# Kernel tuning notes

Measured on AMD Instinct MI355X. Metric: run time of the kernel, lower is better.

## Reference

```python
import jax, jax.numpy as jnp
import numpy as np


def setup_inputs() -> dict:
    key = jax.random.key(0)
    k1, k2, k3 = jax.random.split(key, 3)
    B, C2, H, W = 8, 128, 28, 28   # resnet18 layer2 output for 224x224 input
    C3, H3, W3 = 256, 14, 14       # resnet18 layer3 output
    M = 30000                      # memory bank patches (post-coreset)
    f2 = jax.random.normal(k1, (B, C2, H, W), dtype=jnp.float32)
    f3 = jax.random.normal(k2, (B, C3, H3, W3), dtype=jnp.float32)
    memory_bank = jax.random.normal(k3, (M, C2 + C3), dtype=jnp.float32)
    return {"f2": f2, "f3": f3, "memory_bank": memory_bank}


def reference(f2, f3, memory_bank):
    """PatchCore predict: multi-layer embed + brute-force 1-NN euclidean distance.

    f2: [B,C2,H,W] (layer2 feats), f3: [B,C3,H3,W3] (layer3 feats),
    memory_bank: [M, C2+C3]. Returns (patch_scores [B,H,W], img_scores [B]).
    """
    B, C2, H, W = f2.shape
    C3 = f3.shape[1]
    # F.interpolate(..., mode='bilinear', align_corners=False) == jax.image.resize bilinear
    f3_up = jax.image.resize(f3, (B, C3, H, W), method="bilinear")
    emb = jnp.concatenate([f2, f3_up], axis=1)            # [B,C,H,W], C=C2+C3
    C = C2 + C3
    patches = emb.transpose(0, 2, 3, 1).reshape(-1, C)    # [N,C], N=B*H*W
    x_sq = jnp.sum(patches * patches, axis=-1, keepdims=True)      # [N,1]
    m_sq = jnp.sum(memory_bank * memory_bank, axis=-1)[None, :]    # [1,M]
    d2 = x_sq + m_sq - 2.0 * (patches @ memory_bank.T)             # [N,M]
    dists = jnp.sqrt(jnp.maximum(d2, 1e-12))
    nn_dist = jnp.min(dists, axis=1)                               # 1-NN (n_neighbors=1)
    patch_scores = nn_dist.reshape(B, H, W)
    img_scores = jnp.max(patch_scores.reshape(B, -1), axis=1)
    return patch_scores, img_scores
```

## Files before the change

### kernel.cpp

```cpp
#include <hip/hip_runtime.h>
#include <hip/hip_bf16.h>
#include <stdint.h>

typedef float f32x4 __attribute__((ext_vector_type(4)));
typedef short bf16x8 __attribute__((ext_vector_type(8)));

#define NPATCH 6272
#define CTOT   384
#define MBANK  30000
#define MROWS  6400
#define NCOLS  30208
#define NKT    6

__global__ __launch_bounds__(256) void prep_patches_kernel(
    const float* __restrict__ f2, const float* __restrict__ f3,
    __hip_bfloat16* __restrict__ A, float* __restrict__ x_sq,
    float* __restrict__ nn_d2)
{
  const int lane = threadIdx.x & 63;
  const int n = blockIdx.x * 4 + (threadIdx.x >> 6);
  if (n >= MROWS) return;
  if (n >= NPATCH) {
    #pragma unroll
    for (int j = 0; j < 6; ++j) A[(size_t)n * CTOT + j * 64 + lane] = __float2bfloat16(0.f);
    return;
  }
  const int b = n / 784;
  const int hw = n - b * 784;
  const int h = hw / 28;
  const int w = hw - h * 28;

  int h0, h1, w0i, w1i; float wh0, wh1, ww0, ww1;
  if (h & 1) { int k = h >> 1; h0 = k; h1 = (k + 1 < 14) ? k + 1 : 13; wh0 = 0.75f; wh1 = 0.25f; }
  else       { int k = h >> 1; h0 = (k > 0) ? k - 1 : 0; h1 = k;       wh0 = 0.25f; wh1 = 0.75f; }
  if (w & 1) { int k = w >> 1; w0i = k; w1i = (k + 1 < 14) ? k + 1 : 13; ww0 = 0.75f; ww1 = 0.25f; }
  else       { int k = w >> 1; w0i = (k > 0) ? k - 1 : 0; w1i = k;       ww0 = 0.25f; ww1 = 0.75f; }

  float ssum = 0.f;
  #pragma unroll
  for (int j = 0; j < 6; ++j) {
    const int c = j * 64 + lane;
    float v;
    if (j < 2) {
      v = f2[(((size_t)b * 128 + c) * 28 + h) * 28 + w];
    } else {
      const int c3 = c - 128;
      const float* p = f3 + ((size_t)b * 256 + c3) * 196;
      v = wh0 * (ww0 * p[h0 * 14 + w0i] + ww1 * p[h0 * 14 + w1i]) +
          wh1 * (ww0 * p[h1 * 14 + w0i] + ww1 * p[h1 * 14 + w1i]);
    }
    A[(size_t)n * CTOT + c] = __float2bfloat16(v);
    ssum += v * v;
  }
  #pragma unroll
  for (int off = 32; off; off >>= 1) ssum += __shfl_xor(ssum, off);
  if (lane == 0) { x_sq[n] = ssum; nn_d2[n] = __uint_as_float(0x7f800000u); }
}

__global__ __launch_bounds__(256) void prep_bank_kernel(
    const float* __restrict__ mb, __hip_bfloat16* __restrict__ Bb,
    float* __restrict__ m_sq)
{
  const int lane = threadIdx.x & 63;
  const int m = blockIdx.x * 4 + (threadIdx.x >> 6);
  if (m >= NCOLS) return;
  if (m < MBANK) {
    float ssum = 0.f;
    #pragma unroll
    for (int j = 0; j < 3; ++j) {
      const int c = j * 128 + lane * 2;
      const float2 v = *(const float2*)&mb[(size_t)m * CTOT + c];
      short2 o;
      o.x = (short)__bfloat16_as_ushort(__float2bfloat16(v.x));
      o.y = (short)__bfloat16_as_ushort(__float2bfloat16(v.y));
      *(short2*)&Bb[(size_t)m * CTOT + c] = o;
      ssum += v.x * v.x + v.y * v.y;
    }
    #pragma unroll
    for (int off = 32; off; off >>= 1) ssum += __shfl_xor(ssum, off);
    if (lane == 0) m_sq[m] = ssum;
  } else {
    #pragma unroll
    for (int j = 0; j < 6; ++j) Bb[(size_t)m * CTOT + j * 64 + lane] = __float2bfloat16(0.f);
    if (lane == 0) m_sq[m] = __uint_as_float(0x7f800000u);
  }
}

__device__ __forceinline__ void gl_lds16(const void* g, void* l) {
  __builtin_amdgcn_global_load_lds(
      (const __attribute__((address_space(1))) uint32_t*)g,
      (__attribute__((address_space(3))) uint32_t*)l, 16, 0, 0);
}

__global__ __launch_bounds__(512, 2) void gemm_min_kernel(
    const __hip_bfloat16* __restrict__ A, const __hip_bfloat16* __restrict__ B,
    const float* __restrict__ x_sq, const float* __restrict__ m_sq,
    float* __restrict__ nn_d2)
{
  __shared__ __align__(16) short As[2][256 * 64];
  __shared__ __align__(16) short Bs[2][256 * 64];
  const int tid  = threadIdx.x;
  const int lane = tid & 63;
  const int wid  = tid >> 6;
  const int wr = wid >> 2;
  const int wc = wid & 3;
  const int row0 = blockIdx.y * 256;
  const int col0 = blockIdx.x * 256;

  f32x4 acc[8][4];
  #pragma unroll
  for (int i = 0; i < 8; ++i)
    #pragma unroll
    for (int j = 0; j < 4; ++j) acc[i][j] = (f32x4){0.f, 0.f, 0.f, 0.f};

  auto stage = [&](int kt, int buf) {
    const int k0 = kt * 64;
    #pragma unroll
    for (int j = 0; j < 4; ++j) {
      const int cb = j * 512 + wid * 64;
      const int c  = cb + lane;
      const int r  = c >> 3;
      const int ch = (c & 7) ^ (r & 7);
      gl_lds16(A + (size_t)(row0 + r) * CTOT + k0 + ch * 8, &As[buf][cb * 8]);
      gl_lds16(B + (size_t)(col0 + r) * CTOT + k0 + ch * 8, &Bs[buf][cb * 8]);
    }
  };

  stage(0, 0);
  stage(1, 1);
  asm volatile("s_waitcnt vmcnt(8)" ::: "memory");
  __builtin_amdgcn_s_barrier();

  const int sw = lane & 7;
  const int rA = wr * 128 + (lane & 15);
  const int rB = wc * 64 + (lane & 15);
  const int kq = lane >> 4;

  #pragma unroll
  for (int t = 0; t < NKT; ++t) {
    const int cur = t & 1;
    const short* lA = As[cur];
    const short* lB = Bs[cur];
    const int ch0 = (kq ^ sw) << 4;
    const int ch1 = ((4 + kq) ^ sw) << 4;

    bf16x8 a0[8], b0[4], a1[8], b1[4];
    #pragma unroll
    for (int mi = 0; mi < 8; ++mi)
      a0[mi] = *(const bf16x8*)((const char*)lA + (rA + mi * 16) * 128 + ch0);
    #pragma unroll
    for (int ni = 0; ni < 4; ++ni)
      b0[ni] = *(const bf16x8*)((const char*)lB + (rB + ni * 16) * 128 + ch0);
    #pragma unroll
    for (int mi = 0; mi < 8; ++mi)
      a1[mi] = *(const bf16x8*)((const char*)lA + (rA + mi * 16) * 128 + ch1);
    #pragma unroll
    for (int ni = 0; ni < 4; ++ni)
      b1[ni] = *(const bf16x8*)((const char*)lB + (rB + ni * 16) * 128 + ch1);

    #pragma unroll
    for (int mi = 0; mi < 8; ++mi)
      #pragma unroll
      for (int ni = 0; ni < 4; ++ni)
        acc[mi][ni] = __builtin_amdgcn_mfma_f32_16x16x32_bf16(a0[mi], b0[ni], acc[mi][ni], 0, 0, 0);

    asm volatile("s_waitcnt lgkmcnt(0)" ::: "memory");
    __builtin_amdgcn_s_barrier();
    if (t + 2 < NKT) stage(t + 2, cur);

    __builtin_amdgcn_s_setprio(1);
    #pragma unroll
    for (int mi = 0; mi < 8; ++mi)
      #pragma unroll
      for (int ni = 0; ni < 4; ++ni)
        acc[mi][ni] = __builtin_amdgcn_mfma_f32_16x16x32_bf16(a1[mi], b1[ni], acc[mi][ni], 0, 0, 0);
    __builtin_amdgcn_s_setprio(0);

    if (t + 2 < NKT) {
      asm volatile("s_waitcnt vmcnt(8)" ::: "memory");
    } else {
      asm volatile("s_waitcnt vmcnt(0)" ::: "memory");
    }
    __builtin_amdgcn_s_barrier();
  }

  float msq[4];
  #pragma unroll
  for (int ni = 0; ni < 4; ++ni) msq[ni] = m_sq[col0 + wc * 64 + ni * 16 + (lane & 15)];

  #pragma unroll
  for (int mi = 0; mi < 8; ++mi) {
    #pragma unroll
    for (int r = 0; r < 4; ++r) {
      float t = msq[0] - 2.f * acc[mi][0][r];
      #pragma unroll
      for (int ni = 1; ni < 4; ++ni) t = fminf(t, msq[ni] - 2.f * acc[mi][ni][r]);
      t = fminf(t, __shfl_xor(t, 1));
      t = fminf(t, __shfl_xor(t, 2));
      t = fminf(t, __shfl_xor(t, 4));
      t = fminf(t, __shfl_xor(t, 8));
      if ((lane & 15) == 0) {
        const int rg = row0 + wr * 128 + mi * 16 + ((lane >> 4) << 2) + r;
        if (rg < NPATCH) {
          const float v = fmaxf(t + x_sq[rg], 0.f);
          atomicMin((unsigned int*)&nn_d2[rg], __float_as_uint(v));
        }
      }
    }
  }
}

__global__ __launch_bounds__(256) void finalize_kernel(
    const float* __restrict__ nn_d2, float* __restrict__ out)
{
  const int b = blockIdx.x;
  const int tid = threadIdx.x;
  __shared__ float red[4];
  float lmax = 0.f;
  for (int i = tid; i < 784; i += 256) {
    const float d2 = nn_d2[b * 784 + i];
    const float s = sqrtf(fmaxf(d2, 1e-12f));
    out[b * 784 + i] = s;
    lmax = fmaxf(lmax, s);
  }
  #pragma unroll
  for (int off = 32; off; off >>= 1) lmax = fmaxf(lmax, __shfl_xor(lmax, off));
  if ((tid & 63) == 0) red[tid >> 6] = lmax;
  __syncthreads();
  if (tid == 0)
    out[6272 + b] = fmaxf(fmaxf(red[0], red[1]), fmaxf(red[2], red[3]));
}

extern "C" void kernel_launch(void* const* d_in, const int* in_sizes, int n_in,
                              void* d_out, int out_size, void* d_ws, size_t ws_size,
                              hipStream_t stream)
{
  const float* f2 = (const float*)d_in[0];
  const float* f3 = (const float*)d_in[1];
  const float* mb = (const float*)d_in[2];
  float* out = (float*)d_out;

  uint8_t* ws = (uint8_t*)d_ws;
  __hip_bfloat16* A  = (__hip_bfloat16*)(ws);
  __hip_bfloat16* Bb = (__hip_bfloat16*)(ws + 4915200);
  float* x_sq  = (float*)(ws + 28114944);
  float* m_sq  = (float*)(ws + 28140544);
  float* nn_d2 = (float*)(ws + 28261376);

  hipLaunchKernelGGL(prep_patches_kernel, dim3(MROWS / 4), dim3(256), 0, stream,
                     f2, f3, A, x_sq, nn_d2);
  hipLaunchKernelGGL(prep_bank_kernel, dim3(NCOLS / 4), dim3(256), 0, stream,
                     mb, Bb, m_sq);
  hipLaunchKernelGGL(gemm_min_kernel, dim3(NCOLS / 256, MROWS / 256), dim3(512), 0, stream,
                     A, Bb, x_sq, m_sq, nn_d2);
  hipLaunchKernelGGL(finalize_kernel, dim3(8), dim3(256), 0, stream, nn_d2, out);
}
```

Before: 452.5 us.

## Interleave GEMM tile staging with quarter-phase MFMA blocks and merge prep kernels

```diff
diff --git a/kernel.cpp b/kernel.cpp
--- a/kernel.cpp
+++ b/kernel.cpp
@@ -12,77 +12,78 @@
 #define NCOLS  30208
 #define NKT    6
 
-__global__ __launch_bounds__(256) void prep_patches_kernel(
+#define NPB    (MROWS / 4)
+#define NBB    (NCOLS / 4)
+
+__global__ __launch_bounds__(256) void prep_kernel(
     const float* __restrict__ f2, const float* __restrict__ f3,
-    __hip_bfloat16* __restrict__ A, float* __restrict__ x_sq,
+    const float* __restrict__ mb,
+    __hip_bfloat16* __restrict__ A, __hip_bfloat16* __restrict__ Bb,
+    float* __restrict__ x_sq, float* __restrict__ m_sq,
     float* __restrict__ nn_d2)
 {
   const int lane = threadIdx.x & 63;
-  const int n = blockIdx.x * 4 + (threadIdx.x >> 6);
-  if (n >= MROWS) return;
-  if (n >= NPATCH) {
-    #pragma unroll
-    for (int j = 0; j < 6; ++j) A[(size_t)n * CTOT + j * 64 + lane] = __float2bfloat16(0.f);
-    return;
-  }
-  const int b = n / 784;
-  const int hw = n - b * 784;
-  const int h = hw / 28;
-  const int w = hw - h * 28;
-
-  int h0, h1, w0i, w1i; float wh0, wh1, ww0, ww1;
-  if (h & 1) { int k = h >> 1; h0 = k; h1 = (k + 1 < 14) ? k + 1 : 13; wh0 = 0.75f; wh1 = 0.25f; }
-  else       { int k = h >> 1; h0 = (k > 0) ? k - 1 : 0; h1 = k;       wh0 = 0.25f; wh1 = 0.75f; }
-  if (w & 1) { int k = w >> 1; w0i = k; w1i = (k + 1 < 14) ? k + 1 : 13; ww0 = 0.75f; ww1 = 0.25f; }
-  else       { int k = w >> 1; w0i = (k > 0) ? k - 1 : 0; w1i = k;       ww0 = 0.25f; ww1 = 0.75f; }
-
-  float ssum = 0.f;
-  #pragma unroll
-  for (int j = 0; j < 6; ++j) {
-    const int c = j * 64 + lane;
-    float v;
-    if (j < 2) {
-      v = f2[(((size_t)b * 128 + c) * 28 + h) * 28 + w];
+  const int sub  = threadIdx.x >> 6;
+
+  if (blockIdx.x < NPB) {
+    const int n = blockIdx.x * 4 + sub;
+    if (n >= NPATCH) {
+      #pragma unroll
+      for (int j = 0; j < 6; ++j) A[(size_t)n * CTOT + j * 64 + lane] = __float2bfloat16(0.f);
+      return;
+    }
+    const int b = n / 784;
+    const int hw = n - b * 784;
+    const int h = hw / 28;
+    const int w = hw - h * 28;
+
+    int h0, h1, w0i, w1i; float wh0, wh1, ww0, ww1;
+    if (h & 1) { int k = h >> 1; h0 = k; h1 = (k + 1 < 14) ? k + 1 : 13; wh0 = 0.75f; wh1 = 0.25f; }
+    else       { int k = h >> 1; h0 = (k > 0) ? k - 1 : 0; h1 = k;       wh0 = 0.25f; wh1 = 0.75f; }
+    if (w & 1) { int k = w >> 1; w0i = k; w1i = (k + 1 < 14) ? k + 1 : 13; ww0 = 0.75f; ww1 = 0.25f; }
+    else       { int k = w >> 1; w0i = (k > 0) ? k - 1 : 0; w1i = k;       ww0 = 0.25f; ww1 = 0.75f; }
+
+    float ssum = 0.f;
+    #pragma unroll
+    for (int j = 0; j < 6; ++j) {
+      const int c = j * 64 + lane;
+      float v;
+      if (j < 2) {
+        v = f2[(((size_t)b * 128 + c) * 28 + h) * 28 + w];
+      } else {
+        const int c3 = c - 128;
+        const float* p = f3 + ((size_t)b * 256 + c3) * 196;
+        v = wh0 * (ww0 * p[h0 * 14 + w0i] + ww1 * p[h0 * 14 + w1i]) +
+            wh1 * (ww0 * p[h1 * 14 + w0i] + ww1 * p[h1 * 14 + w1i]);
+      }
+      A[(size_t)n * CTOT + c] = __float2bfloat16(v);
+      ssum += v * v;
+    }
+    #pragma unroll
+    for (int off = 32; off; off >>= 1) ssum += __shfl_xor(ssum, off);
+    if (lane == 0) { x_sq[n] = ssum; nn_d2[n] = __uint_as_float(0x7f800000u); }
+  } else {
+    const int m = (blockIdx.x - NPB) * 4 + sub;
+    if (m < MBANK) {
+      float ssum = 0.f;
+      #pragma unroll
+      for (int j = 0; j < 3; ++j) {
+        const int c = j * 128 + lane * 2;
+        const float2 v = *(const float2*)&mb[(size_t)m * CTOT + c];
+        short2 o;
+        o.x = (short)__bfloat16_as_ushort(__float2bfloat16(v.x));
+        o.y = (short)__bfloat16_as_ushort(__float2bfloat16(v.y));
+        *(short2*)&Bb[(size_t)m * CTOT + c] = o;
+        ssum += v.x * v.x + v.y * v.y;
+      }
+      #pragma unroll
+      for (int off = 32; off; off >>= 1) ssum += __shfl_xor(ssum, off);
+      if (lane == 0) m_sq[m] = ssum;
     } else {
-      const int c3 = c - 128;
-      const float* p = f3 + ((size_t)b * 256 + c3) * 196;
-      v = wh0 * (ww0 * p[h0 * 14 + w0i] + ww1 * p[h0 * 14 + w1i]) +
-          wh1 * (ww0 * p[h1 * 14 + w0i] + ww1 * p[h1 * 14 + w1i]);
-    }
-    A[(size_t)n * CTOT + c] = __float2bfloat16(v);
-    ssum += v * v;
-  }
-  #pragma unroll
-  for (int off = 32; off; off >>= 1) ssum += __shfl_xor(ssum, off);
-  if (lane == 0) { x_sq[n] = ssum; nn_d2[n] = __uint_as_float(0x7f800000u); }
-}
-
-__global__ __launch_bounds__(256) void prep_bank_kernel(
-    const float* __restrict__ mb, __hip_bfloat16* __restrict__ Bb,
-    float* __restrict__ m_sq)
-{
-  const int lane = threadIdx.x & 63;
-  const int m = blockIdx.x * 4 + (threadIdx.x >> 6);
-  if (m >= NCOLS) return;
-  if (m < MBANK) {
-    float ssum = 0.f;
-    #pragma unroll
-    for (int j = 0; j < 3; ++j) {
-      const int c = j * 128 + lane * 2;
-      const float2 v = *(const float2*)&mb[(size_t)m * CTOT + c];
-      short2 o;
-      o.x = (short)__bfloat16_as_ushort(__float2bfloat16(v.x));
-      o.y = (short)__bfloat16_as_ushort(__float2bfloat16(v.y));
-      *(short2*)&Bb[(size_t)m * CTOT + c] = o;
-      ssum += v.x * v.x + v.y * v.y;
-    }
-    #pragma unroll
-    for (int off = 32; off; off >>= 1) ssum += __shfl_xor(ssum, off);
-    if (lane == 0) m_sq[m] = ssum;
-  } else {
-    #pragma unroll
-    for (int j = 0; j < 6; ++j) Bb[(size_t)m * CTOT + j * 64 + lane] = __float2bfloat16(0.f);
-    if (lane == 0) m_sq[m] = __uint_as_float(0x7f800000u);
+      #pragma unroll
+      for (int j = 0; j < 6; ++j) Bb[(size_t)m * CTOT + j * 64 + lane] = __float2bfloat16(0.f);
+      if (lane == 0) m_sq[m] = __uint_as_float(0x7f800000u);
+    }
   }
 }
 
@@ -113,21 +114,20 @@
     #pragma unroll
     for (int j = 0; j < 4; ++j) acc[i][j] = (f32x4){0.f, 0.f, 0.f, 0.f};
 
-  auto stage = [&](int kt, int buf) {
+  auto stage_pair = [&](int kt, int buf, int j) {
     const int k0 = kt * 64;
-    #pragma unroll
-    for (int j = 0; j < 4; ++j) {
-      const int cb = j * 512 + wid * 64;
-      const int c  = cb + lane;
-      const int r  = c >> 3;
-      const int ch = (c & 7) ^ (r & 7);
-      gl_lds16(A + (size_t)(row0 + r) * CTOT + k0 + ch * 8, &As[buf][cb * 8]);
-      gl_lds16(B + (size_t)(col0 + r) * CTOT + k0 + ch * 8, &Bs[buf][cb * 8]);
-    }
+    const int cb = j * 512 + wid * 64;
+    const int c  = cb + lane;
+    const int r  = c >> 3;
+    const int ch = (c & 7) ^ (r & 7);
+    gl_lds16(A + (size_t)(row0 + r) * CTOT + k0 + ch * 8, &As[buf][cb * 8]);
+    gl_lds16(B + (size_t)(col0 + r) * CTOT + k0 + ch * 8, &Bs[buf][cb * 8]);
   };
 
-  stage(0, 0);
-  stage(1, 1);
+  #pragma unroll
+  for (int j = 0; j < 4; ++j) stage_pair(0, 0, j);
+  #pragma unroll
+  for (int j = 0; j < 4; ++j) stage_pair(1, 1, j);
   asm volatile("s_waitcnt vmcnt(8)" ::: "memory");
   __builtin_amdgcn_s_barrier();
 
@@ -135,52 +135,77 @@
   const int rA = wr * 128 + (lane & 15);
   const int rB = wc * 64 + (lane & 15);
   const int kq = lane >> 4;
+  const int ch0 = (kq ^ sw) << 4;
+  const int ch1 = ((4 + kq) ^ sw) << 4;
 
   #pragma unroll
   for (int t = 0; t < NKT; ++t) {
     const int cur = t & 1;
-    const short* lA = As[cur];
-    const short* lB = Bs[cur];
-    const int ch0 = (kq ^ sw) << 4;
-    const int ch1 = ((4 + kq) ^ sw) << 4;
-
+    const char* lA = (const char*)As[cur];
+    const char* lB = (const char*)Bs[cur];
+    const bool st = (t >= 1) && (t + 1 < NKT);
     bf16x8 a0[8], b0[4], a1[8], b1[4];
-    #pragma unroll
-    for (int mi = 0; mi < 8; ++mi)
-      a0[mi] = *(const bf16x8*)((const char*)lA + (rA + mi * 16) * 128 + ch0);
-    #pragma unroll
-    for (int ni = 0; ni < 4; ++ni)
-      b0[ni] = *(const bf16x8*)((const char*)lB + (rB + ni * 16) * 128 + ch0);
-    #pragma unroll
-    for (int mi = 0; mi < 8; ++mi)
-      a1[mi] = *(const bf16x8*)((const char*)lA + (rA + mi * 16) * 128 + ch1);
-    #pragma unroll
-    for (int ni = 0; ni < 4; ++ni)
-      b1[ni] = *(const bf16x8*)((const char*)lB + (rB + ni * 16) * 128 + ch1);
-
-    #pragma unroll
-    for (int mi = 0; mi < 8; ++mi)
+
+    #pragma unroll
+    for (int ni = 0; ni < 4; ++ni) b0[ni] = *(const bf16x8*)(lB + (rB + ni * 16) * 128 + ch0);
+    #pragma unroll
+    for (int mi = 0; mi < 4; ++mi) a0[mi] = *(const bf16x8*)(lA + (rA + mi * 16) * 128 + ch0);
+    if (st) stage_pair(t + 1, cur ^ 1, 0);
+    __builtin_amdgcn_s_barrier();
+    asm volatile("s_waitcnt lgkmcnt(0)" ::: "memory");
+    __builtin_amdgcn_s_setprio(1);
+    #pragma unroll
+    for (int mi = 0; mi < 4; ++mi)
       #pragma unroll
       for (int ni = 0; ni < 4; ++ni)
         acc[mi][ni] = __builtin_amdgcn_mfma_f32_16x16x32_bf16(a0[mi], b0[ni], acc[mi][ni], 0, 0, 0);
-
-    asm volatile("s_waitcnt lgkmcnt(0)" ::: "memory");
-    __builtin_amdgcn_s_barrier();
-    if (t + 2 < NKT) stage(t + 2, cur);
-
-    __builtin_amdgcn_s_setprio(1);
-    #pragma unroll
-    for (int mi = 0; mi < 8; ++mi)
+    __builtin_amdgcn_s_setprio(0);
+    __builtin_amdgcn_s_barrier();
+
+    #pragma unroll
+    for (int mi = 4; mi < 8; ++mi) a0[mi] = *(const bf16x8*)(lA + (rA + mi * 16) * 128 + ch0);
+    if (st) stage_pair(t + 1, cur ^ 1, 1);
+    __builtin_amdgcn_s_barrier();
+    asm volatile("s_waitcnt lgkmcnt(0)" ::: "memory");
+    __builtin_amdgcn_s_setprio(1);
+    #pragma unroll
+    for (int mi = 4; mi < 8; ++mi)
+      #pragma unroll
+      for (int ni = 0; ni < 4; ++ni)
+        acc[mi][ni] = __builtin_amdgcn_mfma_f32_16x16x32_bf16(a0[mi], b0[ni], acc[mi][ni], 0, 0, 0);
+    __builtin_amdgcn_s_setprio(0);
+    __builtin_amdgcn_s_barrier();
+
+    #pragma unroll
+    for (int ni = 0; ni < 4; ++ni) b1[ni] = *(const bf16x8*)(lB + (rB + ni * 16) * 128 + ch1);
+    #pragma unroll
+    for (int mi = 0; mi < 4; ++mi) a1[mi] = *(const bf16x8*)(lA + (rA + mi * 16) * 128 + ch1);
+    if (st) stage_pair(t + 1, cur ^ 1, 2);
+    __builtin_amdgcn_s_barrier();
+    asm volatile("s_waitcnt lgkmcnt(0)" ::: "memory");
+    __builtin_amdgcn_s_setprio(1);
+    #pragma unroll
+    for (int mi = 0; mi < 4; ++mi)
       #pragma unroll
       for (int ni = 0; ni < 4; ++ni)
         acc[mi][ni] = __builtin_amdgcn_mfma_f32_16x16x32_bf16(a1[mi], b1[ni], acc[mi][ni], 0, 0, 0);
     __builtin_amdgcn_s_setprio(0);
-
-    if (t + 2 < NKT) {
-      asm volatile("s_waitcnt vmcnt(8)" ::: "memory");
-    } else {
+    __builtin_amdgcn_s_barrier();
+
+    #pragma unroll
+    for (int mi = 4; mi < 8; ++mi) a1[mi] = *(const bf16x8*)(lA + (rA + mi * 16) * 128 + ch1);
+    if (st) stage_pair(t + 1, cur ^ 1, 3);
+    __builtin_amdgcn_s_barrier();
+    asm volatile("s_waitcnt lgkmcnt(0)" ::: "memory");
+    __builtin_amdgcn_s_setprio(1);
+    #pragma unroll
+    for (int mi = 4; mi < 8; ++mi)
+      #pragma unroll
+      for (int ni = 0; ni < 4; ++ni)
+        acc[mi][ni] = __builtin_amdgcn_mfma_f32_16x16x32_bf16(a1[mi], b1[ni], acc[mi][ni], 0, 0, 0);
+    __builtin_amdgcn_s_setprio(0);
+    if (t + 1 < NKT)
       asm volatile("s_waitcnt vmcnt(0)" ::: "memory");
-    }
     __builtin_amdgcn_s_barrier();
   }
 
@@ -247,10 +272,8 @@
   float* m_sq  = (float*)(ws + 28140544);
   float* nn_d2 = (float*)(ws + 28261376);
 
-  hipLaunchKernelGGL(prep_patches_kernel, dim3(MROWS / 4), dim3(256), 0, stream,
-                     f2, f3, A, x_sq, nn_d2);
-  hipLaunchKernelGGL(prep_bank_kernel, dim3(NCOLS / 4), dim3(256), 0, stream,
-                     mb, Bb, m_sq);
+  hipLaunchKernelGGL(prep_kernel, dim3(NPB + NBB), dim3(256), 0, stream,
+                     f2, f3, mb, A, Bb, x_sq, m_sq, nn_d2);
   hipLaunchKernelGGL(gemm_min_kernel, dim3(NCOLS / 256, MROWS / 256), dim3(512), 0, stream,
                      A, Bb, x_sq, m_sq, nn_d2);
   hipLaunchKernelGGL(finalize_kernel, dim3(8), dim3(256), 0, stream, nn_d2, out);
```

Result: slower. 468.4 us (+3.5%).
